# Kernel tuning notes

Measured on AMD Instinct MI355X. Metric: run time of the kernel, lower is better.

Reference implementation:

```python
import jax, jax.numpy as jnp
import numpy as np

N, E, G = 60000, 240000, 1024   # nodes, edges, batched graphs
H, Dh = 4, 32                   # num_heads, hidden_dim
HD = H * Dh
FN, FE = 17, 15                 # raw node/edge feature dims
LAYERS = 3                      # cfg.EGAT_layers


def setup_inputs() -> dict:
    key = jax.random.key(0)
    ks = iter(jax.random.split(key, 64))
    def nrm(shape, s=0.05):
        return jax.random.normal(next(ks), shape, dtype=jnp.float32) * s
    def zeros(shape):
        return jnp.zeros(shape, jnp.float32)
    inp = {
        'hR': nrm((N, FN), 1.0), 'eR': nrm((E, FE), 1.0),
        'hP': nrm((N, FN), 1.0), 'eP': nrm((E, FE), 1.0),
        'srcR': jax.random.randint(next(ks), (E,), 0, N, dtype=jnp.int32),
        'dstR': jax.random.randint(next(ks), (E,), 0, N, dtype=jnp.int32),
        'srcP': jax.random.randint(next(ks), (E,), 0, N, dtype=jnp.int32),
        'dstP': jax.random.randint(next(ks), (E,), 0, N, dtype=jnp.int32),
        'nid': jnp.sort(jax.random.randint(next(ks), (N,), 0, G, dtype=jnp.int32)),
        'eid': jnp.sort(jax.random.randint(next(ks), (E,), 0, G, dtype=jnp.int32)),
        # egat1 (DGL EGATConv): in_node=17, in_edge=15 -> H*Dh
        'W1_ni': nrm((FN, HD)), 'b1_ni': zeros((HD,)),
        'W1_nj': nrm((FN, HD)), 'b1_nj': zeros((HD,)),
        'W1_f': nrm((FE, HD)), 'b1_f': zeros((HD,)),
        'W1_node': nrm((FN, HD)), 'b1_node': zeros((HD,)),
        'attn1': nrm((H, Dh), 0.1),
        # egat2: in_node=in_edge=HD -> H*Dh
        'W2_ni': nrm((HD, HD)), 'b2_ni': zeros((HD,)),
        'W2_nj': nrm((HD, HD)), 'b2_nj': zeros((HD,)),
        'W2_f': nrm((HD, HD)), 'b2_f': zeros((HD,)),
        'W2_node': nrm((HD, HD)), 'b2_node': zeros((HD,)),
        'attn2': nrm((H, Dh), 0.1),
        # aggregation linears
        'Wa_n': nrm((HD, HD)), 'ba_n': zeros((HD,)),
        'Wa_e': nrm((HD, HD)), 'ba_e': zeros((HD,)),
        # MLP head
        'Wm1': nrm((2 * HD, 512)), 'bm1': zeros((512,)),
        'Wm2': nrm((512, 256)), 'bm2': zeros((256,)),
        'Wm3': nrm((256, 1)), 'bm3': zeros((1,)),
    }
    return inp


def egat_layer(h, e, src, dst, Wni, bni, Wnj, bnj, Wf, bf, Wnode, bnode, attn):
    """DGL EGATConv: gather-attend-scatter with edge-softmax over dst."""
    n_edges = src.shape[0]
    f_ni = h @ Wni + bni                      # [N, HD]
    f_nj = h @ Wnj + bnj                      # [N, HD]
    f_out = jax.nn.leaky_relu(f_ni[src] + f_nj[dst] + e @ Wf + bf, 0.01)
    f_out = f_out.reshape(n_edges, H, Dh)     # [E, H, Dh]
    logits = jnp.einsum('ehd,hd->eh', f_out, attn)  # [E, H]
    m = jax.lax.stop_gradient(jax.ops.segment_max(logits, dst, num_segments=N))
    ex = jnp.exp(logits - m[dst])
    denom = jax.ops.segment_sum(ex, dst, num_segments=N)
    a = ex / denom[dst]                       # [E, H] edge softmax
    h_node = (h @ Wnode + bnode).reshape(N, H, Dh)
    msg = h_node[src] * a[:, :, None]         # [E, H, Dh]
    h_out = jax.ops.segment_sum(msg, dst, num_segments=N)
    return h_out.reshape(N, HD), f_out.reshape(n_edges, HD)


def reference(hR, eR, hP, eP, srcR, dstR, srcP, dstP, nid, eid,
              W1_ni, b1_ni, W1_nj, b1_nj, W1_f, b1_f, W1_node, b1_node, attn1,
              W2_ni, b2_ni, W2_nj, b2_nj, W2_f, b2_f, W2_node, b2_node, attn2,
              Wa_n, ba_n, Wa_e, ba_e, Wm1, bm1, Wm2, bm2, Wm3, bm3):
    # egat1 on reactant and product graphs
    hRn, eRn = egat_layer(hR, eR, srcR, dstR, W1_ni, b1_ni, W1_nj, b1_nj,
                          W1_f, b1_f, W1_node, b1_node, attn1)
    hPn, ePn = egat_layer(hP, eP, srcP, dstP, W1_ni, b1_ni, W1_nj, b1_nj,
                          W1_f, b1_f, W1_node, b1_node, attn1)
    # EGAT_layers-1 rounds of egat2 on R; source recomputes egat1(P) each
    # iteration, which is identical to the value above, so P is unchanged.
    for _ in range(LAYERS - 1):
        hRn, eRn = egat_layer(hRn, eRn, srcR, dstR, W2_ni, b2_ni, W2_nj, b2_nj,
                              W2_f, b2_f, W2_node, b2_node, attn2)
    # Aggregate == 'Diff' branch
    rxn_node = (hPn - hRn) @ Wa_n + ba_n      # [N, HD]
    rxn_edge = (ePn - eRn) @ Wa_e + ba_e      # [E, HD]
    # dgl.unbatch + per-graph sum == segment_sum by graph id
    Gn = jax.ops.segment_sum(rxn_node, nid, num_segments=G)   # [G, HD]
    Ge = jax.ops.segment_sum(rxn_edge, eid, num_segments=G)   # [G, HD]
    Gf = jnp.concatenate([Gn, Ge], axis=1)    # [G, 2*HD]
    x = jax.nn.relu(Gf @ Wm1 + bm1)
    x = jax.nn.relu(x @ Wm2 + bm2)
    x = x @ Wm3 + bm3                         # [G, 1]
    return x
```

## Files before the change

kernel.cpp:

```cpp
#include <hip/hip_runtime.h>
#include <cstddef>
#include <cstdint>

typedef unsigned int uint;
typedef unsigned short ushort;
typedef __attribute__((ext_vector_type(4))) float f32x4;
typedef __attribute__((ext_vector_type(8))) short short8;

__device__ __forceinline__ ushort f2b(float v) {
  uint x = __float_as_uint(v);
  return (ushort)((x + 0x7fffu + ((x >> 16) & 1u)) >> 16);
}
__device__ __forceinline__ float b2f_lo(uint u) { return __uint_as_float(u << 16); }
__device__ __forceinline__ float b2f_hi(uint u) { return __uint_as_float(u & 0xffff0000u); }
__device__ __forceinline__ float ld1(const float* p) { return *p; }
__device__ __forceinline__ float ld1(const ushort* p) { return __uint_as_float(((uint)*p) << 16); }
__device__ __forceinline__ void st1(float* p, float v) { *p = v; }
__device__ __forceinline__ void st1(ushort* p, float v) { *p = f2b(v); }

__device__ __forceinline__ uint4 ldA8(const float* p) {
  float4 a = *(const float4*)p;
  float4 b = *(const float4*)(p + 4);
  uint4 r;
  r.x = (uint)f2b(a.x) | ((uint)f2b(a.y) << 16);
  r.y = (uint)f2b(a.z) | ((uint)f2b(a.w) << 16);
  r.z = (uint)f2b(b.x) | ((uint)f2b(b.y) << 16);
  r.w = (uint)f2b(b.z) | ((uint)f2b(b.w) << 16);
  return r;
}
__device__ __forceinline__ uint4 ldA8(const ushort* p) { return *(const uint4*)p; }

__device__ __forceinline__ int lowerb(const int* __restrict__ ids, int M, int v) {
  int lo = 0, hi = M;
  while (lo < hi) { int mid = (lo + hi) >> 1; if (ids[mid] < v) lo = mid + 1; else hi = mid; }
  return lo;
}

__global__ void fillzi(int* p, int n) {
  int i = blockIdx.x * 256 + threadIdx.x;
  if (i < n) p[i] = 0;
}
__global__ void fillzf(float* p, int n) {
  int i = blockIdx.x * 256 + threadIdx.x;
  if (i < n) p[i] = 0.f;
}

__global__ void hist_dst(const int* __restrict__ dst, int* __restrict__ cnt, int E) {
  int e = blockIdx.x * 256 + threadIdx.x;
  if (e < E) atomicAdd(&cnt[dst[e]], 1);
}

__global__ void scan_local(const int* __restrict__ cnt, int* __restrict__ rowptr,
                           int* __restrict__ blocksum, int N) {
  __shared__ int tmp[256];
  int t = threadIdx.x;
  int i = blockIdx.x * 256 + t;
  int v = (i < N) ? cnt[i] : 0;
  tmp[t] = v;
  __syncthreads();
  for (int ofs = 1; ofs < 256; ofs <<= 1) {
    int u = (t >= ofs) ? tmp[t - ofs] : 0;
    __syncthreads();
    tmp[t] += u;
    __syncthreads();
  }
  if (i < N) rowptr[i] = tmp[t] - v;
  if (t == 255) blocksum[blockIdx.x] = tmp[255];
}

__global__ void scan_block(int* __restrict__ bs, int n) {
  __shared__ int tmp[256];
  int t = threadIdx.x;
  int v = (t < n) ? bs[t] : 0;
  tmp[t] = v;
  __syncthreads();
  for (int ofs = 1; ofs < 256; ofs <<= 1) {
    int u = (t >= ofs) ? tmp[t - ofs] : 0;
    __syncthreads();
    tmp[t] += u;
    __syncthreads();
  }
  if (t < n) bs[t] = tmp[t] - v;
}

__global__ void scan_add(int* __restrict__ rowptr, int* __restrict__ cursor,
                         const int* __restrict__ blocksum, int N, int E) {
  int i = blockIdx.x * 256 + threadIdx.x;
  if (i < N) {
    int v = rowptr[i] + blocksum[blockIdx.x];
    rowptr[i] = v;
    cursor[i] = v;
  }
  if (i == 0) rowptr[N] = E;
}

__global__ void scatter_idx(const int* __restrict__ dst, const int* __restrict__ src,
                            int* __restrict__ cursor,
                            int* __restrict__ eperm, int* __restrict__ invperm,
                            int* __restrict__ src_perm, int E) {
  int e = blockIdx.x * 256 + threadIdx.x;
  if (e < E) {
    int p = atomicAdd(&cursor[dst[e]], 1);
    eperm[p] = e;
    invperm[e] = p;
    src_perm[p] = src[e];
  }
}

__global__ void prep_w(const float* __restrict__ W, ushort* __restrict__ Wt) {
  int t = threadIdx.x;
  int n = t >> 1;
  int k0 = (t & 1) * 64;
  uint sw = (uint)(n & 7) << 3;
  for (int kk = 0; kk < 64; ++kk) {
    int k = k0 + kk;
    Wt[n * 128 + (k ^ sw)] = f2b(W[k * 128 + n]);
  }
}

template<typename TIn, typename TOut>
__global__ __launch_bounds__(256) void gemm_k128(const TIn* X, int ldx,
                                                 const ushort* __restrict__ Wt,
                                                 const float* __restrict__ b,
                                                 TOut* Y, int ldy, int M) {
  __shared__ ushort As[128 * 128];
  __shared__ ushort Bs[128 * 128];
  int t = threadIdx.x;
  int row0 = blockIdx.x * 128;

  {
    const uint4* s4 = (const uint4*)Wt + t * 8;
    uint4* d4 = (uint4*)Bs + t * 8;
#pragma unroll
    for (int c = 0; c < 8; ++c) d4[c] = s4[c];
  }
  {
    int r = t >> 1;
    int k0h = (t & 1) * 64;
    int grow = row0 + r;
    uint sw = (uint)(r & 7) << 3;
    if (grow < M) {
      const TIn* xr = X + (size_t)grow * ldx;
#pragma unroll
      for (int c = 0; c < 8; ++c) {
        int k0 = k0h + c * 8;
        *(uint4*)(As + r * 128 + (k0 ^ sw)) = ldA8(xr + k0);
      }
    } else {
      uint4 z = make_uint4(0, 0, 0, 0);
#pragma unroll
      for (int c = 0; c < 8; ++c) {
        int k0 = k0h + c * 8;
        *(uint4*)(As + r * 128 + (k0 ^ sw)) = z;
      }
    }
  }
  __syncthreads();

  int lane = t & 63;
  int wid = t >> 6;
  int wr = wid >> 1, wc = wid & 1;
  uint swl = (uint)(lane & 7) << 3;

  f32x4 acc[4][4];
#pragma unroll
  for (int n4 = 0; n4 < 4; ++n4) {
    float bv = b[wc * 64 + n4 * 16 + (lane & 15)];
#pragma unroll
    for (int m4 = 0; m4 < 4; ++m4) acc[m4][n4] = (f32x4){bv, bv, bv, bv};
  }

#pragma unroll
  for (int kk = 0; kk < 4; ++kk) {
    int kidx = kk * 32 + 8 * (lane >> 4);
    short8 af[4], bfr[4];
#pragma unroll
    for (int m4 = 0; m4 < 4; ++m4) {
      int rm = wr * 64 + m4 * 16 + (lane & 15);
      af[m4] = *(const short8*)(As + rm * 128 + (kidx ^ swl));
    }
#pragma unroll
    for (int n4 = 0; n4 < 4; ++n4) {
      int cn = wc * 64 + n4 * 16 + (lane & 15);
      bfr[n4] = *(const short8*)(Bs + cn * 128 + (kidx ^ swl));
    }
#pragma unroll
    for (int m4 = 0; m4 < 4; ++m4)
#pragma unroll
      for (int n4 = 0; n4 < 4; ++n4)
        acc[m4][n4] = __builtin_amdgcn_mfma_f32_16x16x32_bf16(af[m4], bfr[n4], acc[m4][n4], 0, 0, 0);
  }

  int coln = wc * 64 + (lane & 15);
#pragma unroll
  for (int m4 = 0; m4 < 4; ++m4) {
    int rb = row0 + wr * 64 + m4 * 16 + ((lane >> 4) << 2);
#pragma unroll
    for (int n4 = 0; n4 < 4; ++n4) {
      int cc = coln + n4 * 16;
#pragma unroll
      for (int i = 0; i < 4; ++i)
        if (rb + i < M) st1(Y + (size_t)(rb + i) * ldy + cc, acc[m4][n4][i]);
    }
  }
}

__global__ __launch_bounds__(256) void gemm3_k128(
    const ushort* __restrict__ X,
    const ushort* __restrict__ Wt0, const float* __restrict__ b0, ushort* __restrict__ Y0, int ldy0,
    const ushort* __restrict__ Wt1, const float* __restrict__ b1, ushort* __restrict__ Y1, int ldy1,
    const ushort* __restrict__ Wt2, const float* __restrict__ b2, ushort* __restrict__ Y2, int ldy2,
    int M) {
  __shared__ ushort As[128 * 128];
  __shared__ ushort Bs[128 * 128];
  int t = threadIdx.x;
  int row0 = blockIdx.x * 128;

  {
    int r = t >> 1;
    int k0h = (t & 1) * 64;
    int grow = row0 + r;
    uint sw = (uint)(r & 7) << 3;
    if (grow < M) {
      const ushort* xr = X + (size_t)grow * 128;
#pragma unroll
      for (int c = 0; c < 8; ++c) {
        int k0 = k0h + c * 8;
        *(uint4*)(As + r * 128 + (k0 ^ sw)) = *(const uint4*)(xr + k0);
      }
    } else {
      uint4 z = make_uint4(0, 0, 0, 0);
#pragma unroll
      for (int c = 0; c < 8; ++c) {
        int k0 = k0h + c * 8;
        *(uint4*)(As + r * 128 + (k0 ^ sw)) = z;
      }
    }
  }

  int lane = t & 63;
  int wid = t >> 6;
  int wr = wid >> 1, wc = wid & 1;
  uint swl = (uint)(lane & 7) << 3;

#pragma unroll
  for (int w = 0; w < 3; ++w) {
    const ushort* Wt = (w == 0) ? Wt0 : (w == 1) ? Wt1 : Wt2;
    const float* bb  = (w == 0) ? b0  : (w == 1) ? b1  : b2;
    ushort* Y        = (w == 0) ? Y0  : (w == 1) ? Y1  : Y2;
    int ldy          = (w == 0) ? ldy0 : (w == 1) ? ldy1 : ldy2;

    if (w > 0) __syncthreads();
    {
      const uint4* s4 = (const uint4*)Wt + t * 8;
      uint4* d4 = (uint4*)Bs + t * 8;
#pragma unroll
      for (int c = 0; c < 8; ++c) d4[c] = s4[c];
    }
    __syncthreads();

    f32x4 acc[4][4];
#pragma unroll
    for (int n4 = 0; n4 < 4; ++n4) {
      float bv = bb[wc * 64 + n4 * 16 + (lane & 15)];
#pragma unroll
      for (int m4 = 0; m4 < 4; ++m4) acc[m4][n4] = (f32x4){bv, bv, bv, bv};
    }
#pragma unroll
    for (int kk = 0; kk < 4; ++kk) {
      int kidx = kk * 32 + 8 * (lane >> 4);
      short8 af[4], bfr[4];
#pragma unroll
      for (int m4 = 0; m4 < 4; ++m4) {
        int rm = wr * 64 + m4 * 16 + (lane & 15);
        af[m4] = *(const short8*)(As + rm * 128 + (kidx ^ swl));
      }
#pragma unroll
      for (int n4 = 0; n4 < 4; ++n4) {
        int cn = wc * 64 + n4 * 16 + (lane & 15);
        bfr[n4] = *(const short8*)(Bs + cn * 128 + (kidx ^ swl));
      }
#pragma unroll
      for (int m4 = 0; m4 < 4; ++m4)
#pragma unroll
        for (int n4 = 0; n4 < 4; ++n4)
          acc[m4][n4] = __builtin_amdgcn_mfma_f32_16x16x32_bf16(af[m4], bfr[n4], acc[m4][n4], 0, 0, 0);
    }
    int coln = wc * 64 + (lane & 15);
#pragma unroll
    for (int m4 = 0; m4 < 4; ++m4) {
      int rb = row0 + wr * 64 + m4 * 16 + ((lane >> 4) << 2);
#pragma unroll
      for (int n4 = 0; n4 < 4; ++n4) {
        int cc = coln + n4 * 16;
#pragma unroll
        for (int i = 0; i < 4; ++i)
          if (rb + i < M) Y[(size_t)(rb + i) * ldy + cc] = f2b(acc[m4][n4][i]);
      }
    }
  }
}

template<int K>
__global__ __launch_bounds__(128) void lin3_small(const float* __restrict__ X,
    const float* __restrict__ W1, const float* __restrict__ b1,
    const float* __restrict__ W2, const float* __restrict__ b2,
    const float* __restrict__ W3, const float* __restrict__ b3,
    ushort* __restrict__ Ynin, ushort* __restrict__ Ynj, int M) {
  constexpr int ROWS = 16;
  __shared__ float xs[ROWS * K];
  int t = threadIdx.x;
  int row0 = blockIdx.x * ROWS;
  int nr = M - row0; if (nr > ROWS) nr = ROWS;
  for (int i = t; i < nr * K; i += 128) xs[i] = X[(size_t)row0 * K + i];
  __syncthreads();
  float a1[ROWS], a2[ROWS], a3[ROWS];
  float v1 = b1[t], v2 = b2[t], v3 = b3[t];
#pragma unroll
  for (int r = 0; r < ROWS; ++r) { a1[r] = v1; a2[r] = v2; a3[r] = v3; }
#pragma unroll
  for (int k = 0; k < K; ++k) {
    float w1 = W1[k * 128 + t], w2 = W2[k * 128 + t], w3 = W3[k * 128 + t];
#pragma unroll
    for (int r = 0; r < ROWS; ++r) {
      float x = xs[r * K + k];
      a1[r] = fmaf(x, w1, a1[r]);
      a2[r] = fmaf(x, w2, a2[r]);
      a3[r] = fmaf(x, w3, a3[r]);
    }
  }
  for (int r = 0; r < nr; ++r) {
    size_t n = (size_t)(row0 + r);
    Ynin[n * 256 + t] = f2b(a1[r]);
    Ynin[n * 256 + 128 + t] = f2b(a3[r]);
    Ynj[n * 128 + t] = f2b(a2[r]);
  }
}

template<int K>
__global__ __launch_bounds__(128) void lin1_perm(const float* __restrict__ X,
    const float* __restrict__ W, const float* __restrict__ b,
    const int* __restrict__ eperm, ushort* __restrict__ Y, int M) {
  constexpr int ROWS = 16;
  __shared__ float xs[ROWS * K];
  __shared__ int es[ROWS];
  int t = threadIdx.x;
  int row0 = blockIdx.x * ROWS;
  int nr = M - row0; if (nr > ROWS) nr = ROWS;
  if (t < nr) es[t] = eperm[row0 + t];
  __syncthreads();
  for (int i = t; i < nr * K; i += 128) {
    int r = i / K, c = i - r * K;
    xs[i] = X[(size_t)es[r] * K + c];
  }
  __syncthreads();
  float acc[ROWS];
  float bias = b[t];
#pragma unroll
  for (int r = 0; r < ROWS; ++r) acc[r] = bias;
#pragma unroll
  for (int k = 0; k < K; ++k) {
    float w = W[k * 128 + t];
#pragma unroll
    for (int r = 0; r < ROWS; ++r) acc[r] = fmaf(xs[r * K + k], w, acc[r]);
  }
  for (int r = 0; r < nr; ++r) Y[(size_t)(row0 + r) * 128 + t] = f2b(acc[r]);
}

__global__ void egat_gather(const ushort* __restrict__ f_nin,
                            const ushort* __restrict__ f_nj,
                            ushort* ebp,
                            const int* __restrict__ src_perm,
                            const int* __restrict__ rowptr,
                            const float* __restrict__ attn,
                            ushort* __restrict__ nb, int N) {
  int d = blockIdx.x * 4 + (threadIdx.x >> 6);
  if (d >= N) return;
  int lane = threadIdx.x & 63;
  int lo = rowptr[d], hi = rowptr[d + 1];
  int h = lane >> 4;
  float2 at = *(const float2*)(attn + h * 32 + (lane & 15) * 2);
  uint unj = *((const uint*)(f_nj + (size_t)d * 128) + lane);
  float nj0 = b2f_lo(unj), nj1 = b2f_hi(unj);
  float acc0 = 0.f, acc1 = 0.f, exsum = 0.f;
  for (int i = lo; i < hi; ++i) {
    int s = src_perm[i];
    const uint* pn = (const uint*)(f_nin + (size_t)s * 256);
    uint uni = pn[lane];
    uint und = pn[64 + lane];
    uint* ep = (uint*)(ebp + (size_t)i * 128) + lane;
    uint ue = *ep;
    float v0 = b2f_lo(ue) + b2f_lo(uni) + nj0;
    float v1 = b2f_hi(ue) + b2f_hi(uni) + nj1;
    v0 = v0 >= 0.f ? v0 : 0.01f * v0;
    v1 = v1 >= 0.f ? v1 : 0.01f * v1;
    *ep = (uint)f2b(v0) | ((uint)f2b(v1) << 16);
    float p = v0 * at.x + v1 * at.y;
    p += __shfl_xor(p, 1);
    p += __shfl_xor(p, 2);
    p += __shfl_xor(p, 4);
    p += __shfl_xor(p, 8);
    float ev = __expf(p);
    exsum += ev;
    acc0 = fmaf(b2f_lo(und), ev, acc0);
    acc1 = fmaf(b2f_hi(und), ev, acc1);
  }
  float inv = exsum > 0.f ? 1.f / exsum : 0.f;
  ((uint*)(nb + (size_t)d * 128))[lane] =
      (uint)f2b(acc0 * inv) | ((uint)f2b(acc1 * inv) << 16);
}

template<int ROWS>
__global__ __launch_bounds__(256) void segsum_bf16(const ushort* __restrict__ X,
    const int* __restrict__ ids, int M, float* __restrict__ S) {
  int r0 = (blockIdx.x * 4 + (threadIdx.x >> 6)) * ROWS;
  if (r0 >= M) return;
  int r1 = r0 + ROWS; if (r1 > M) r1 = M;
  int t = threadIdx.x & 63;
  float a0 = 0.f, a1 = 0.f;
  int cur = ids[r0];
  for (int r = r0; r < r1; ++r) {
    int id = ids[r];
    if (id != cur) {
      atomicAdd(&S[(size_t)cur * 128 + 2 * t], a0);
      atomicAdd(&S[(size_t)cur * 128 + 2 * t + 1], a1);
      a0 = a1 = 0.f; cur = id;
    }
    uint u = *((const uint*)(X + (size_t)r * 128) + t);
    a0 += b2f_lo(u); a1 += b2f_hi(u);
  }
  atomicAdd(&S[(size_t)cur * 128 + 2 * t], a0);
  atomicAdd(&S[(size_t)cur * 128 + 2 * t + 1], a1);
}

template<int ROWS>
__global__ __launch_bounds__(256) void segsum_bf16g(const ushort* __restrict__ X,
    const int* __restrict__ invperm,
    const int* __restrict__ ids, int M, float* __restrict__ S) {
  int r0 = (blockIdx.x * 4 + (threadIdx.x >> 6)) * ROWS;
  if (r0 >= M) return;
  int r1 = r0 + ROWS; if (r1 > M) r1 = M;
  int t = threadIdx.x & 63;
  float a0 = 0.f, a1 = 0.f;
  int cur = ids[r0];
  for (int r = r0; r < r1; ++r) {
    int id = ids[r];
    if (id != cur) {
      atomicAdd(&S[(size_t)cur * 128 + 2 * t], a0);
      atomicAdd(&S[(size_t)cur * 128 + 2 * t + 1], a1);
      a0 = a1 = 0.f; cur = id;
    }
    uint u = *((const uint*)(X + (size_t)invperm[r] * 128) + t);
    a0 += b2f_lo(u); a1 += b2f_hi(u);
  }
  atomicAdd(&S[(size_t)cur * 128 + 2 * t], a0);
  atomicAdd(&S[(size_t)cur * 128 + 2 * t + 1], a1);
}

__global__ void seg_cnt(const int* __restrict__ ids, int M, int* __restrict__ cnt, int G) {
  int g = blockIdx.x * 256 + threadIdx.x;
  if (g < G) cnt[g] = lowerb(ids, M, g + 1) - lowerb(ids, M, g);
}

__global__ void diff_linear(const float* __restrict__ SP, const float* __restrict__ SR,
                            const int* __restrict__ cnt,
                            const float* __restrict__ W, const float* __restrict__ b,
                            float* __restrict__ out, int ldo, int coloff) {
  int g = blockIdx.x;
  int t = threadIdx.x;
  __shared__ float xs[128];
  xs[t] = SP[(size_t)g * 128 + t] - SR[(size_t)g * 128 + t];
  __syncthreads();
  float acc = (float)cnt[g] * b[t];
  for (int k = 0; k < 128; ++k) acc = fmaf(xs[k], W[k * 128 + t], acc);
  out[(size_t)g * ldo + coloff + t] = acc;
}

template<int K, int NC, bool RELU>
__global__ void mlp_linear(const float* __restrict__ X, const float* __restrict__ W,
                           const float* __restrict__ b, float* __restrict__ Y) {
  int g = blockIdx.x;
  int t = threadIdx.x;
  __shared__ float xs[K];
  for (int i = t; i < K; i += NC) xs[i] = X[(size_t)g * K + i];
  __syncthreads();
  float acc = b[t];
  for (int k = 0; k < K; ++k) acc = fmaf(xs[k], W[k * NC + t], acc);
  if (RELU) acc = fmaxf(acc, 0.f);
  Y[(size_t)g * NC + t] = acc;
}

__global__ void mlp_final(const float* __restrict__ X, const float* __restrict__ W,
                          const float* __restrict__ b, float* __restrict__ out, int G) {
  int g = blockIdx.x * blockDim.x + threadIdx.x;
  if (g >= G) return;
  float acc = b[0];
  for (int k = 0; k < 256; ++k) acc = fmaf(X[(size_t)g * 256 + k], W[k], acc);
  out[g] = acc;
}

struct LayerW {
  const float *Wni, *bni, *Wnj, *bnj, *Wf, *bf, *Wnode, *bnode, *attn;
};

extern "C" void kernel_launch(void* const* d_in, const int* in_sizes, int n_in,
                              void* d_out, int out_size, void* d_ws, size_t ws_size,
                              hipStream_t stream) {
  const float* hR = (const float*)d_in[0];
  const float* eR = (const float*)d_in[1];
  const float* hP = (const float*)d_in[2];
  const float* eP = (const float*)d_in[3];
  const int* srcR = (const int*)d_in[4];
  const int* dstR = (const int*)d_in[5];
  const int* srcP = (const int*)d_in[6];
  const int* dstP = (const int*)d_in[7];
  const int* nid  = (const int*)d_in[8];
  const int* eid  = (const int*)d_in[9];
  LayerW w1 { (const float*)d_in[10], (const float*)d_in[11], (const float*)d_in[12],
              (const float*)d_in[13], (const float*)d_in[14], (const float*)d_in[15],
              (const float*)d_in[16], (const float*)d_in[17], (const float*)d_in[18] };
  LayerW w2 { (const float*)d_in[19], (const float*)d_in[20], (const float*)d_in[21],
              (const float*)d_in[22], (const float*)d_in[23], (const float*)d_in[24],
              (const float*)d_in[25], (const float*)d_in[26], (const float*)d_in[27] };
  const float* Wa_n = (const float*)d_in[28];
  const float* ba_n = (const float*)d_in[29];
  const float* Wa_e = (const float*)d_in[30];
  const float* ba_e = (const float*)d_in[31];
  const float* Wm1  = (const float*)d_in[32];
  const float* bm1  = (const float*)d_in[33];
  const float* Wm2  = (const float*)d_in[34];
  const float* bm2  = (const float*)d_in[35];
  const float* Wm3  = (const float*)d_in[36];
  const float* bm3  = (const float*)d_in[37];

  const int N = in_sizes[0] / 17;
  const int E = in_sizes[4];
  const int G = out_size;

  char* base = (char*)d_ws;
  size_t off = 0;
  auto alloc = [&](size_t bytes) { char* p = base + off; off += (bytes + 255) & ~(size_t)255; return p; };
  ushort* nb     = (ushort*)alloc((size_t)N * 128 * 2);
  ushort* f_nin  = (ushort*)alloc((size_t)N * 256 * 2);
  ushort* f_nj   = (ushort*)alloc((size_t)N * 128 * 2);
  ushort* ebp    = (ushort*)alloc((size_t)E * 128 * 2);
  int*    rowptrP = (int*)alloc((size_t)(N + 1) * 4);
  int*    rowptrR = (int*)alloc((size_t)(N + 1) * 4);
  int*    epermP  = (int*)alloc((size_t)E * 4);
  int*    epermR  = (int*)alloc((size_t)E * 4);
  int*    invpermP = (int*)alloc((size_t)E * 4);
  int*    invpermR = (int*)alloc((size_t)E * 4);
  int*    srcpermP = (int*)alloc((size_t)E * 4);
  int*    srcpermR = (int*)alloc((size_t)E * 4);
  int*    cnt     = (int*)alloc((size_t)N * 4);
  int*    cursor  = (int*)alloc((size_t)N * 4);
  int*    blocksum = (int*)alloc(1024 * 4);
  ushort* Wt_ni  = (ushort*)alloc(128 * 128 * 2);
  ushort* Wt_nj  = (ushort*)alloc(128 * 128 * 2);
  ushort* Wt_f   = (ushort*)alloc(128 * 128 * 2);
  ushort* Wt_nd  = (ushort*)alloc(128 * 128 * 2);
  float*  SnP    = (float*)alloc((size_t)G * 128 * 4);
  float*  SnR    = (float*)alloc((size_t)G * 128 * 4);
  float*  SeP    = (float*)alloc((size_t)G * 128 * 4);
  float*  SeR    = (float*)alloc((size_t)G * 128 * 4);
  float*  Gf     = (float*)alloc((size_t)G * 256 * 4);
  float*  x1     = (float*)alloc((size_t)G * 512 * 4);
  float*  x2     = (float*)alloc((size_t)G * 256 * 4);
  int*    cnt_n  = (int*)alloc((size_t)G * 4);
  int*    cnt_e  = (int*)alloc((size_t)G * 4);
  if (off > ws_size) return;

  const int EB = (E + 255) / 256;
  const int NB = (N + 255) / 256;

  fillzf<<<(G * 512 + 255) / 256, 256, 0, stream>>>(SnP, G * 512);

  auto build_csr = [&](const int* dst, const int* src, int* rowptr,
                       int* eperm, int* invperm, int* src_perm) {
    fillzi<<<NB, 256, 0, stream>>>(cnt, N);
    hist_dst<<<EB, 256, 0, stream>>>(dst, cnt, E);
    scan_local<<<NB, 256, 0, stream>>>(cnt, rowptr, blocksum, N);
    scan_block<<<1, 256, 0, stream>>>(blocksum, NB);
    scan_add<<<NB, 256, 0, stream>>>(rowptr, cursor, blocksum, N, E);
    scatter_idx<<<EB, 256, 0, stream>>>(dst, src, cursor, eperm, invperm, src_perm, E);
  };
  build_csr(dstP, srcP, rowptrP, epermP, invpermP, srcpermP);
  build_csr(dstR, srcR, rowptrR, epermR, invpermR, srcpermR);

  prep_w<<<1, 256, 0, stream>>>(w2.Wni,   Wt_ni);
  prep_w<<<1, 256, 0, stream>>>(w2.Wnj,   Wt_nj);
  prep_w<<<1, 256, 0, stream>>>(w2.Wf,    Wt_f);
  prep_w<<<1, 256, 0, stream>>>(w2.Wnode, Wt_nd);

  seg_cnt<<<(G + 255) / 256, 256, 0, stream>>>(nid, N, cnt_n, G);
  seg_cnt<<<(G + 255) / 256, 256, 0, stream>>>(eid, E, cnt_e, G);

  const int GB = (N + 3) / 4;

  auto layer1 = [&](const float* h, const float* e, const int* eperm,
                    const int* src_perm, const int* rowptr) {
    lin3_small<17><<<(N + 15) / 16, 128, 0, stream>>>(h, w1.Wni, w1.bni, w1.Wnj, w1.bnj,
                                                      w1.Wnode, w1.bnode, f_nin, f_nj, N);
    lin1_perm<15><<<(E + 15) / 16, 128, 0, stream>>>(e, w1.Wf, w1.bf, eperm, ebp, E);
    egat_gather<<<GB, 256, 0, stream>>>(f_nin, f_nj, ebp, src_perm, rowptr, w1.attn, nb, N);
  };
  auto layer2 = [&](const int* src_perm, const int* rowptr) {
    gemm3_k128<<<(N + 127) / 128, 256, 0, stream>>>(nb,
        Wt_ni, w2.bni,   f_nin,       256,
        Wt_nd, w2.bnode, f_nin + 128, 256,
        Wt_nj, w2.bnj,   f_nj,        128, N);
    gemm_k128<ushort, ushort><<<(E + 127) / 128, 256, 0, stream>>>(ebp, 128, Wt_f, w2.bf, ebp, 128, E);
    egat_gather<<<GB, 256, 0, stream>>>(f_nin, f_nj, ebp, src_perm, rowptr, w2.attn, nb, N);
  };

  layer1(hP, eP, epermP, srcpermP, rowptrP);
  segsum_bf16<32><<<(N + 127) / 128, 256, 0, stream>>>(nb, nid, N, SnP);
  segsum_bf16g<16><<<(E + 63) / 64, 256, 0, stream>>>(ebp, invpermP, eid, E, SeP);

  layer1(hR, eR, epermR, srcpermR, rowptrR);
  layer2(srcpermR, rowptrR);
  layer2(srcpermR, rowptrR);
  segsum_bf16<32><<<(N + 127) / 128, 256, 0, stream>>>(nb, nid, N, SnR);
  segsum_bf16g<16><<<(E + 63) / 64, 256, 0, stream>>>(ebp, invpermR, eid, E, SeR);

  diff_linear<<<G, 128, 0, stream>>>(SnP, SnR, cnt_n, Wa_n, ba_n, Gf, 256, 0);
  diff_linear<<<G, 128, 0, stream>>>(SeP, SeR, cnt_e, Wa_e, ba_e, Gf, 256, 128);

  mlp_linear<256, 512, true><<<G, 512, 0, stream>>>(Gf, Wm1, bm1, x1);
  mlp_linear<512, 256, true><<<G, 256, 0, stream>>>(x1, Wm2, bm2, x2);
  mlp_final<<<(G + 255) / 256, 256, 0, stream>>>(x2, Wm3, bm3, (float*)d_out, G);
}
```

Measured before the change: 713.3 us.

## Fuse edge linear with node-feature add, LeakyReLU and attention logits

The edge feature computation (the layer-1 small linear and the layer-2 128x128 GEMM) now also gathers the source and destination node projections, applies LeakyReLU, writes the edge output and computes exp(attention logits) into a per-edge buffer. The gather kernel then only reads these exponentials and the source node features for the softmax-weighted sum, so it no longer re-reads and rewrites the edge tensor. The four weight-prep launches are merged into one. In exchange the code adds a dst_perm index array, an extra E*4 float buffer, smaller 64-row GEMM tiles that read the weights directly from global memory, and node-row gathers inside the GEMM.

```diff
diff --git a/kernel.cpp b/kernel.cpp
--- a/kernel.cpp
+++ b/kernel.cpp
@@ -11,24 +11,9 @@
   uint x = __float_as_uint(v);
   return (ushort)((x + 0x7fffu + ((x >> 16) & 1u)) >> 16);
 }
+__device__ __forceinline__ float b2f(ushort u) { return __uint_as_float(((uint)u) << 16); }
 __device__ __forceinline__ float b2f_lo(uint u) { return __uint_as_float(u << 16); }
 __device__ __forceinline__ float b2f_hi(uint u) { return __uint_as_float(u & 0xffff0000u); }
-__device__ __forceinline__ float ld1(const float* p) { return *p; }
-__device__ __forceinline__ float ld1(const ushort* p) { return __uint_as_float(((uint)*p) << 16); }
-__device__ __forceinline__ void st1(float* p, float v) { *p = v; }
-__device__ __forceinline__ void st1(ushort* p, float v) { *p = f2b(v); }
-
-__device__ __forceinline__ uint4 ldA8(const float* p) {
-  float4 a = *(const float4*)p;
-  float4 b = *(const float4*)(p + 4);
-  uint4 r;
-  r.x = (uint)f2b(a.x) | ((uint)f2b(a.y) << 16);
-  r.y = (uint)f2b(a.z) | ((uint)f2b(a.w) << 16);
-  r.z = (uint)f2b(b.x) | ((uint)f2b(b.y) << 16);
-  r.w = (uint)f2b(b.z) | ((uint)f2b(b.w) << 16);
-  return r;
-}
-__device__ __forceinline__ uint4 ldA8(const ushort* p) { return *(const uint4*)p; }
 
 __device__ __forceinline__ int lowerb(const int* __restrict__ ids, int M, int v) {
   int lo = 0, hi = M;
@@ -97,111 +82,31 @@
 __global__ void scatter_idx(const int* __restrict__ dst, const int* __restrict__ src,
                             int* __restrict__ cursor,
                             int* __restrict__ eperm, int* __restrict__ invperm,
-                            int* __restrict__ src_perm, int E) {
+                            int* __restrict__ src_perm, int* __restrict__ dst_perm, int E) {
   int e = blockIdx.x * 256 + threadIdx.x;
   if (e < E) {
-    int p = atomicAdd(&cursor[dst[e]], 1);
+    int d = dst[e];
+    int p = atomicAdd(&cursor[d], 1);
     eperm[p] = e;
     invperm[e] = p;
     src_perm[p] = src[e];
-  }
-}
-
-__global__ void prep_w(const float* __restrict__ W, ushort* __restrict__ Wt) {
+    dst_perm[p] = d;
+  }
+}
+
+__global__ void prep_w4(const float* __restrict__ W0, const float* __restrict__ W1,
+                        const float* __restrict__ W2, const float* __restrict__ W3,
+                        ushort* __restrict__ T0, ushort* __restrict__ T1,
+                        ushort* __restrict__ T2, ushort* __restrict__ T3) {
+  const float* W = (blockIdx.x == 0) ? W0 : (blockIdx.x == 1) ? W1 : (blockIdx.x == 2) ? W2 : W3;
+  ushort* T      = (blockIdx.x == 0) ? T0 : (blockIdx.x == 1) ? T1 : (blockIdx.x == 2) ? T2 : T3;
   int t = threadIdx.x;
   int n = t >> 1;
   int k0 = (t & 1) * 64;
   uint sw = (uint)(n & 7) << 3;
   for (int kk = 0; kk < 64; ++kk) {
     int k = k0 + kk;
-    Wt[n * 128 + (k ^ sw)] = f2b(W[k * 128 + n]);
-  }
-}
-
-template<typename TIn, typename TOut>
-__global__ __launch_bounds__(256) void gemm_k128(const TIn* X, int ldx,
-                                                 const ushort* __restrict__ Wt,
-                                                 const float* __restrict__ b,
-                                                 TOut* Y, int ldy, int M) {
-  __shared__ ushort As[128 * 128];
-  __shared__ ushort Bs[128 * 128];
-  int t = threadIdx.x;
-  int row0 = blockIdx.x * 128;
-
-  {
-    const uint4* s4 = (const uint4*)Wt + t * 8;
-    uint4* d4 = (uint4*)Bs + t * 8;
-#pragma unroll
-    for (int c = 0; c < 8; ++c) d4[c] = s4[c];
-  }
-  {
-    int r = t >> 1;
-    int k0h = (t & 1) * 64;
-    int grow = row0 + r;
-    uint sw = (uint)(r & 7) << 3;
-    if (grow < M) {
-      const TIn* xr = X + (size_t)grow * ldx;
-#pragma unroll
-      for (int c = 0; c < 8; ++c) {
-        int k0 = k0h + c * 8;
-        *(uint4*)(As + r * 128 + (k0 ^ sw)) = ldA8(xr + k0);
-      }
-    } else {
-      uint4 z = make_uint4(0, 0, 0, 0);
-#pragma unroll
-      for (int c = 0; c < 8; ++c) {
-        int k0 = k0h + c * 8;
-        *(uint4*)(As + r * 128 + (k0 ^ sw)) = z;
-      }
-    }
-  }
-  __syncthreads();
-
-  int lane = t & 63;
-  int wid = t >> 6;
-  int wr = wid >> 1, wc = wid & 1;
-  uint swl = (uint)(lane & 7) << 3;
-
-  f32x4 acc[4][4];
-#pragma unroll
-  for (int n4 = 0; n4 < 4; ++n4) {
-    float bv = b[wc * 64 + n4 * 16 + (lane & 15)];
-#pragma unroll
-    for (int m4 = 0; m4 < 4; ++m4) acc[m4][n4] = (f32x4){bv, bv, bv, bv};
-  }
-
-#pragma unroll
-  for (int kk = 0; kk < 4; ++kk) {
-    int kidx = kk * 32 + 8 * (lane >> 4);
-    short8 af[4], bfr[4];
-#pragma unroll
-    for (int m4 = 0; m4 < 4; ++m4) {
-      int rm = wr * 64 + m4 * 16 + (lane & 15);
-      af[m4] = *(const short8*)(As + rm * 128 + (kidx ^ swl));
-    }
-#pragma unroll
-    for (int n4 = 0; n4 < 4; ++n4) {
-      int cn = wc * 64 + n4 * 16 + (lane & 15);
-      bfr[n4] = *(const short8*)(Bs + cn * 128 + (kidx ^ swl));
-    }
-#pragma unroll
-    for (int m4 = 0; m4 < 4; ++m4)
-#pragma unroll
-      for (int n4 = 0; n4 < 4; ++n4)
-        acc[m4][n4] = __builtin_amdgcn_mfma_f32_16x16x32_bf16(af[m4], bfr[n4], acc[m4][n4], 0, 0, 0);
-  }
-
-  int coln = wc * 64 + (lane & 15);
-#pragma unroll
-  for (int m4 = 0; m4 < 4; ++m4) {
-    int rb = row0 + wr * 64 + m4 * 16 + ((lane >> 4) << 2);
-#pragma unroll
-    for (int n4 = 0; n4 < 4; ++n4) {
-      int cc = coln + n4 * 16;
-#pragma unroll
-      for (int i = 0; i < 4; ++i)
-        if (rb + i < M) st1(Y + (size_t)(rb + i) * ldy + cc, acc[m4][n4][i]);
-    }
+    T[n * 128 + (k ^ sw)] = f2b(W[k * 128 + n]);
   }
 }
 
@@ -301,6 +206,120 @@
   }
 }
 
+static constexpr int NST = 136;
+__global__ __launch_bounds__(256) void gemm_edge_fused(
+    ushort* ebp, const ushort* __restrict__ Wt, const float* __restrict__ b,
+    const ushort* __restrict__ f_nin, const ushort* __restrict__ f_nj,
+    const int* __restrict__ src_perm, const int* __restrict__ dst_perm,
+    const float* __restrict__ attn, float* __restrict__ ex, int E) {
+  __shared__ ushort As[64 * 128];
+  __shared__ ushort Ni[64 * NST];
+  __shared__ ushort Nj[64 * NST];
+  int t = threadIdx.x;
+  int row0 = blockIdx.x * 64;
+
+  {
+    int r = t >> 2, q = t & 3;
+    int grow = row0 + r;
+    uint sw = (uint)(r & 7) << 3;
+    if (grow < E) {
+      const ushort* xr = ebp + (size_t)grow * 128;
+      int s = src_perm[grow], d = dst_perm[grow];
+      const ushort* nir = f_nin + (size_t)s * 256;
+      const ushort* njr = f_nj + (size_t)d * 128;
+#pragma unroll
+      for (int c = 0; c < 4; ++c) {
+        int k0 = q * 32 + c * 8;
+        *(uint4*)(As + r * 128 + (k0 ^ sw)) = *(const uint4*)(xr + k0);
+        *(uint4*)(Ni + r * NST + k0) = *(const uint4*)(nir + k0);
+        *(uint4*)(Nj + r * NST + k0) = *(const uint4*)(njr + k0);
+      }
+    } else {
+      uint4 z = make_uint4(0, 0, 0, 0);
+#pragma unroll
+      for (int c = 0; c < 4; ++c) {
+        int k0 = q * 32 + c * 8;
+        *(uint4*)(As + r * 128 + (k0 ^ sw)) = z;
+      }
+    }
+  }
+  __syncthreads();
+
+  int lane = t & 63;
+  int wid = t >> 6;
+  int wr = wid >> 1, wc = wid & 1;
+  uint swl = (uint)(lane & 7) << 3;
+
+  f32x4 acc[2][4];
+#pragma unroll
+  for (int n4 = 0; n4 < 4; ++n4) {
+    float bv = b[wc * 64 + n4 * 16 + (lane & 15)];
+#pragma unroll
+    for (int m4 = 0; m4 < 2; ++m4) acc[m4][n4] = (f32x4){bv, bv, bv, bv};
+  }
+#pragma unroll
+  for (int kk = 0; kk < 4; ++kk) {
+    int kidx = kk * 32 + 8 * (lane >> 4);
+    short8 af[2], bfr[4];
+#pragma unroll
+    for (int m4 = 0; m4 < 2; ++m4) {
+      int rm = wr * 32 + m4 * 16 + (lane & 15);
+      af[m4] = *(const short8*)(As + rm * 128 + (kidx ^ swl));
+    }
+#pragma unroll
+    for (int n4 = 0; n4 < 4; ++n4) {
+      int cn = wc * 64 + n4 * 16 + (lane & 15);
+      bfr[n4] = *(const short8*)(Wt + cn * 128 + (kidx ^ swl));
+    }
+#pragma unroll
+    for (int m4 = 0; m4 < 2; ++m4)
+#pragma unroll
+      for (int n4 = 0; n4 < 4; ++n4)
+        acc[m4][n4] = __builtin_amdgcn_mfma_f32_16x16x32_bf16(af[m4], bfr[n4], acc[m4][n4], 0, 0, 0);
+  }
+  __syncthreads();
+  float* logits = (float*)As;
+
+  float at4[4];
+#pragma unroll
+  for (int n4 = 0; n4 < 4; ++n4) at4[n4] = attn[wc * 64 + n4 * 16 + (lane & 15)];
+
+#pragma unroll
+  for (int m4 = 0; m4 < 2; ++m4) {
+#pragma unroll
+    for (int i = 0; i < 4; ++i) {
+      int row = wr * 32 + m4 * 16 + ((lane >> 4) << 2) + i;
+      int grow = row0 + row;
+      float ph0 = 0.f, ph1 = 0.f;
+      if (grow < E) {
+#pragma unroll
+        for (int n4 = 0; n4 < 4; ++n4) {
+          int col = wc * 64 + n4 * 16 + (lane & 15);
+          float v = acc[m4][n4][i] + b2f(Ni[row * NST + col]) + b2f(Nj[row * NST + col]);
+          v = v >= 0.f ? v : 0.01f * v;
+          ebp[(size_t)grow * 128 + col] = f2b(v);
+          float p = v * at4[n4];
+          if (n4 < 2) ph0 += p; else ph1 += p;
+        }
+      }
+      ph0 += __shfl_xor(ph0, 1); ph0 += __shfl_xor(ph0, 2);
+      ph0 += __shfl_xor(ph0, 4); ph0 += __shfl_xor(ph0, 8);
+      ph1 += __shfl_xor(ph1, 1); ph1 += __shfl_xor(ph1, 2);
+      ph1 += __shfl_xor(ph1, 4); ph1 += __shfl_xor(ph1, 8);
+      if ((lane & 15) == 0) {
+        logits[row * 4 + wc * 2 + 0] = ph0;
+        logits[row * 4 + wc * 2 + 1] = ph1;
+      }
+    }
+  }
+  __syncthreads();
+  {
+    int row = t >> 2, h = t & 3;
+    int grow = row0 + row;
+    if (grow < E) ex[(size_t)grow * 4 + h] = __expf(logits[row * 4 + h]);
+  }
+}
+
 template<int K>
 __global__ __launch_bounds__(128) void lin3_small(const float* __restrict__ X,
     const float* __restrict__ W1, const float* __restrict__ b1,
@@ -338,21 +357,37 @@
 }
 
 template<int K>
-__global__ __launch_bounds__(128) void lin1_perm(const float* __restrict__ X,
+__global__ __launch_bounds__(128) void lin1_fused(const float* __restrict__ X,
     const float* __restrict__ W, const float* __restrict__ b,
-    const int* __restrict__ eperm, ushort* __restrict__ Y, int M) {
+    const int* __restrict__ eperm, const int* __restrict__ src_perm,
+    const int* __restrict__ dst_perm,
+    const ushort* __restrict__ f_nin, const ushort* __restrict__ f_nj,
+    const float* __restrict__ attn,
+    ushort* __restrict__ Y, float* __restrict__ ex, int M) {
   constexpr int ROWS = 16;
   __shared__ float xs[ROWS * K];
-  __shared__ int es[ROWS];
+  __shared__ int es[ROWS], sS[ROWS], sD[ROWS];
+  __shared__ ushort sNi[ROWS * 128];
+  __shared__ ushort sNj[ROWS * 128];
+  __shared__ float logits[ROWS * 4];
   int t = threadIdx.x;
   int row0 = blockIdx.x * ROWS;
   int nr = M - row0; if (nr > ROWS) nr = ROWS;
-  if (t < nr) es[t] = eperm[row0 + t];
+  if (t < nr) {
+    es[t] = eperm[row0 + t];
+    sS[t] = src_perm[row0 + t];
+    sD[t] = dst_perm[row0 + t];
+  }
   __syncthreads();
   for (int i = t; i < nr * K; i += 128) {
     int r = i / K, c = i - r * K;
     xs[i] = X[(size_t)es[r] * K + c];
   }
+  for (int idx = t; idx < nr * 16; idx += 128) {
+    int r = idx >> 4, c8 = (idx & 15) * 8;
+    *(uint4*)(sNi + r * 128 + c8) = *(const uint4*)(f_nin + (size_t)sS[r] * 256 + c8);
+    *(uint4*)(sNj + r * 128 + c8) = *(const uint4*)(f_nj + (size_t)sD[r] * 128 + c8);
+  }
   __syncthreads();
   float acc[ROWS];
   float bias = b[t];
@@ -364,43 +399,39 @@
 #pragma unroll
     for (int r = 0; r < ROWS; ++r) acc[r] = fmaf(xs[r * K + k], w, acc[r]);
   }
-  for (int r = 0; r < nr; ++r) Y[(size_t)(row0 + r) * 128 + t] = f2b(acc[r]);
-}
-
-__global__ void egat_gather(const ushort* __restrict__ f_nin,
-                            const ushort* __restrict__ f_nj,
-                            ushort* ebp,
-                            const int* __restrict__ src_perm,
-                            const int* __restrict__ rowptr,
-                            const float* __restrict__ attn,
-                            ushort* __restrict__ nb, int N) {
+  float at = attn[t];
+  int lane = t & 63;
+  for (int r = 0; r < nr; ++r) {
+    float v = acc[r] + b2f(sNi[r * 128 + t]) + b2f(sNj[r * 128 + t]);
+    v = v >= 0.f ? v : 0.01f * v;
+    Y[(size_t)(row0 + r) * 128 + t] = f2b(v);
+    float p = v * at;
+    p += __shfl_xor(p, 1); p += __shfl_xor(p, 2);
+    p += __shfl_xor(p, 4); p += __shfl_xor(p, 8); p += __shfl_xor(p, 16);
+    if ((lane & 31) == 0) logits[r * 4 + (t >> 5)] = p;
+  }
+  __syncthreads();
+  if (t < nr * 4) {
+    int r = t >> 2, h = t & 3;
+    ex[(size_t)(row0 + r) * 4 + h] = __expf(logits[r * 4 + h]);
+  }
+}
+
+__global__ void egat_gather2(const ushort* __restrict__ f_nin,
+                             const float* __restrict__ ex,
+                             const int* __restrict__ src_perm,
+                             const int* __restrict__ rowptr,
+                             ushort* __restrict__ nb, int N) {
   int d = blockIdx.x * 4 + (threadIdx.x >> 6);
   if (d >= N) return;
   int lane = threadIdx.x & 63;
   int lo = rowptr[d], hi = rowptr[d + 1];
   int h = lane >> 4;
-  float2 at = *(const float2*)(attn + h * 32 + (lane & 15) * 2);
-  uint unj = *((const uint*)(f_nj + (size_t)d * 128) + lane);
-  float nj0 = b2f_lo(unj), nj1 = b2f_hi(unj);
   float acc0 = 0.f, acc1 = 0.f, exsum = 0.f;
   for (int i = lo; i < hi; ++i) {
+    float ev = ex[(size_t)i * 4 + h];
     int s = src_perm[i];
-    const uint* pn = (const uint*)(f_nin + (size_t)s * 256);
-    uint uni = pn[lane];
-    uint und = pn[64 + lane];
-    uint* ep = (uint*)(ebp + (size_t)i * 128) + lane;
-    uint ue = *ep;
-    float v0 = b2f_lo(ue) + b2f_lo(uni) + nj0;
-    float v1 = b2f_hi(ue) + b2f_hi(uni) + nj1;
-    v0 = v0 >= 0.f ? v0 : 0.01f * v0;
-    v1 = v1 >= 0.f ? v1 : 0.01f * v1;
-    *ep = (uint)f2b(v0) | ((uint)f2b(v1) << 16);
-    float p = v0 * at.x + v1 * at.y;
-    p += __shfl_xor(p, 1);
-    p += __shfl_xor(p, 2);
-    p += __shfl_xor(p, 4);
-    p += __shfl_xor(p, 8);
-    float ev = __expf(p);
+    uint und = *((const uint*)(f_nin + (size_t)s * 256 + 128) + lane);
     exsum += ev;
     acc0 = fmaf(b2f_lo(und), ev, acc0);
     acc1 = fmaf(b2f_hi(und), ev, acc1);
@@ -544,6 +575,7 @@
   ushort* f_nin  = (ushort*)alloc((size_t)N * 256 * 2);
   ushort* f_nj   = (ushort*)alloc((size_t)N * 128 * 2);
   ushort* ebp    = (ushort*)alloc((size_t)E * 128 * 2);
+  float*  ex     = (float*)alloc((size_t)E * 4 * 4);
   int*    rowptrP = (int*)alloc((size_t)(N + 1) * 4);
   int*    rowptrR = (int*)alloc((size_t)(N + 1) * 4);
   int*    epermP  = (int*)alloc((size_t)E * 4);
@@ -552,6 +584,8 @@
   int*    invpermR = (int*)alloc((size_t)E * 4);
   int*    srcpermP = (int*)alloc((size_t)E * 4);
   int*    srcpermR = (int*)alloc((size_t)E * 4);
+  int*    dstpermP = (int*)alloc((size_t)E * 4);
+  int*    dstpermR = (int*)alloc((size_t)E * 4);
   int*    cnt     = (int*)alloc((size_t)N * 4);
   int*    cursor  = (int*)alloc((size_t)N * 4);
   int*    blocksum = (int*)alloc(1024 * 4);
@@ -576,21 +610,18 @@
   fillzf<<<(G * 512 + 255) / 256, 256, 0, stream>>>(SnP, G * 512);
 
   auto build_csr = [&](const int* dst, const int* src, int* rowptr,
-                       int* eperm, int* invperm, int* src_perm) {
+                       int* eperm, int* invperm, int* src_perm, int* dst_perm) {
     fillzi<<<NB, 256, 0, stream>>>(cnt, N);
     hist_dst<<<EB, 256, 0, stream>>>(dst, cnt, E);
     scan_local<<<NB, 256, 0, stream>>>(cnt, rowptr, blocksum, N);
     scan_block<<<1, 256, 0, stream>>>(blocksum, NB);
     scan_add<<<NB, 256, 0, stream>>>(rowptr, cursor, blocksum, N, E);
-    scatter_idx<<<EB, 256, 0, stream>>>(dst, src, cursor, eperm, invperm, src_perm, E);
+    scatter_idx<<<EB, 256, 0, stream>>>(dst, src, cursor, eperm, invperm, src_perm, dst_perm, E);
   };
-  build_csr(dstP, srcP, rowptrP, epermP, invpermP, srcpermP);
-  build_csr(dstR, srcR, rowptrR, epermR, invpermR, srcpermR);
-
-  prep_w<<<1, 256, 0, stream>>>(w2.Wni,   Wt_ni);
-  prep_w<<<1, 256, 0, stream>>>(w2.Wnj,   Wt_nj);
-  prep_w<<<1, 256, 0, stream>>>(w2.Wf,    Wt_f);
-  prep_w<<<1, 256, 0, stream>>>(w2.Wnode, Wt_nd);
+  build_csr(dstP, srcP, rowptrP, epermP, invpermP, srcpermP, dstpermP);
+  build_csr(dstR, srcR, rowptrR, epermR, invpermR, srcpermR, dstpermR);
+
+  prep_w4<<<4, 256, 0, stream>>>(w2.Wni, w2.Wnj, w2.Wf, w2.Wnode, Wt_ni, Wt_nj, Wt_f, Wt_nd);
 
   seg_cnt<<<(G + 255) / 256, 256, 0, stream>>>(nid, N, cnt_n, G);
   seg_cnt<<<(G + 255) / 256, 256, 0, stream>>>(eid, E, cnt_e, G);
@@ -598,28 +629,30 @@
   const int GB = (N + 3) / 4;
 
   auto layer1 = [&](const float* h, const float* e, const int* eperm,
-                    const int* src_perm, const int* rowptr) {
+                    const int* src_perm, const int* dst_perm, const int* rowptr) {
     lin3_small<17><<<(N + 15) / 16, 128, 0, stream>>>(h, w1.Wni, w1.bni, w1.Wnj, w1.bnj,
                                                       w1.Wnode, w1.bnode, f_nin, f_nj, N);
-    lin1_perm<15><<<(E + 15) / 16, 128, 0, stream>>>(e, w1.Wf, w1.bf, eperm, ebp, E);
-    egat_gather<<<GB, 256, 0, stream>>>(f_nin, f_nj, ebp, src_perm, rowptr, w1.attn, nb, N);
+    lin1_fused<15><<<(E + 15) / 16, 128, 0, stream>>>(e, w1.Wf, w1.bf, eperm, src_perm,
+                                                      dst_perm, f_nin, f_nj, w1.attn, ebp, ex, E);
+    egat_gather2<<<GB, 256, 0, stream>>>(f_nin, ex, src_perm, rowptr, nb, N);
   };
-  auto layer2 = [&](const int* src_perm, const int* rowptr) {
+  auto layer2 = [&](const int* src_perm, const int* dst_perm, const int* rowptr) {
     gemm3_k128<<<(N + 127) / 128, 256, 0, stream>>>(nb,
         Wt_ni, w2.bni,   f_nin,       256,
         Wt_nd, w2.bnode, f_nin + 128, 256,
         Wt_nj, w2.bnj,   f_nj,        128, N);
-    gemm_k128<ushort, ushort><<<(E + 127) / 128, 256, 0, stream>>>(ebp, 128, Wt_f, w2.bf, ebp, 128, E);
-    egat_gather<<<GB, 256, 0, stream>>>(f_nin, f_nj, ebp, src_perm, rowptr, w2.attn, nb, N);
+    gemm_edge_fused<<<(E + 63) / 64, 256, 0, stream>>>(ebp, Wt_f, w2.bf, f_nin, f_nj,
+                                                       src_perm, dst_perm, w2.attn, ex, E);
+    egat_gather2<<<GB, 256, 0, stream>>>(f_nin, ex, src_perm, rowptr, nb, N);
   };
 
-  layer1(hP, eP, epermP, srcpermP, rowptrP);
+  layer1(hP, eP, epermP, srcpermP, dstpermP, rowptrP);
   segsum_bf16<32><<<(N + 127) / 128, 256, 0, stream>>>(nb, nid, N, SnP);
   segsum_bf16g<16><<<(E + 63) / 64, 256, 0, stream>>>(ebp, invpermP, eid, E, SeP);
 
-  layer1(hR, eR, epermR, srcpermR, rowptrR);
-  layer2(srcpermR, rowptrR);
-  layer2(srcpermR, rowptrR);
+  layer1(hR, eR, epermR, srcpermR, dstpermR, rowptrR);
+  layer2(srcpermR, dstpermR, rowptrR);
+  layer2(srcpermR, dstpermR, rowptrR);
   segsum_bf16<32><<<(N + 127) / 128, 256, 0, stream>>>(nb, nid, N, SnR);
   segsum_bf16g<16><<<(E + 63) / 64, 256, 0, stream>>>(ebp, invpermR, eid, E, SeR);
 
```

New measurement: 736.7 us. +3.3%, slower.
